# Kernel optimization log

Hardware: AMD Instinct MI355X
Metric: run time of the kernel (lower is better)

The kernel has to match this reference:

```python
import jax, jax.numpy as jnp
import numpy as np

LOG2 = float(np.log(2.0))

def ssp(x):
    # shifted softplus: softplus(x) - log(2)
    return jax.nn.softplus(x) - LOG2

N_NODES = 50000
N_EDGES = 600000
HID = 128
NF = 128

def setup_inputs() -> dict:
    key = jax.random.key(0)
    ks = jax.random.split(key, 10)
    x = jax.random.normal(ks[0], (N_NODES, HID), dtype=jnp.float32)
    edge_attr = jax.random.normal(ks[1], (N_EDGES, NF), dtype=jnp.float32)
    edge_index = jax.random.randint(ks[2], (2, N_EDGES), 0, N_NODES, dtype=jnp.int32)
    s = 1.0 / np.sqrt(NF)
    fc1_w = jax.random.uniform(ks[3], (NF, HID), jnp.float32, -s, s)   # CFConv.fc1 (no bias)
    f_w1 = jax.random.uniform(ks[4], (NF, NF), jnp.float32, -s, s)     # filter_mlp[0]
    f_b1 = jnp.zeros((NF,), jnp.float32)
    f_w2 = jax.random.uniform(ks[5], (NF, NF), jnp.float32, -s, s)     # filter_mlp[2]
    f_b2 = jnp.zeros((NF,), jnp.float32)
    s_w1 = jax.random.uniform(ks[6], (NF, NF), jnp.float32, -s, s)     # StateMLP.fc1
    s_w2 = jax.random.uniform(ks[7], (NF, NF), jnp.float32, -s, s)     # StateMLP.fc2
    return {"x": x, "edge_attr": edge_attr, "edge_index": edge_index,
            "fc1_w": fc1_w, "f_w1": f_w1, "f_b1": f_b1, "f_w2": f_w2,
            "f_b2": f_b2, "s_w1": s_w1, "s_w2": s_w2}

def reference(x, edge_attr, edge_index, fc1_w, f_w1, f_b1, f_w2, f_b2, s_w1, s_w2):
    src, dst = edge_index[0], edge_index[1]  # x_j = x[src], aggregate at dst
    # filter network on edge attributes: [E, NF]
    W = ssp(ssp(edge_attr @ f_w1.T + f_b1) @ f_w2.T + f_b2)
    # message: gather source nodes, linear transform, filter multiply
    msg = (x[src] @ fc1_w.T) * W                               # [E, NF]
    # scatter-add aggregation into nodes
    agg = jax.ops.segment_sum(msg, dst, num_segments=x.shape[0])  # [N, NF]
    # StateMLP
    return ssp(agg @ s_w1.T) @ s_w2.T
```

## Files before the change

kernel.cpp:

```cpp
#include <hip/hip_runtime.h>

#define F 128

typedef __attribute__((ext_vector_type(8))) __bf16 bf16x8;
typedef __attribute__((ext_vector_type(4))) float floatx4;

__device__ __forceinline__ float ssp(float x) {
    return __logf(fmaf(0.5f, __expf(x), 0.5f));
}

__global__ void prep_kernel(const float* __restrict__ fc1w,
                            const float* __restrict__ fw1,
                            const float* __restrict__ fw2,
                            const float* __restrict__ sw1,
                            const float* __restrict__ sw2,
                            __bf16* __restrict__ fc1h, __bf16* __restrict__ fc1l,
                            __bf16* __restrict__ fw1h, __bf16* __restrict__ fw2h,
                            __bf16* __restrict__ sw1h, __bf16* __restrict__ sw1l,
                            __bf16* __restrict__ sw2h, __bf16* __restrict__ sw2l)
{
    int i = blockIdx.x * blockDim.x + threadIdx.x;
    if (i >= F * F) return;
    float v; __bf16 h;
    v = fc1w[i]; h = (__bf16)v; fc1h[i] = h; fc1l[i] = (__bf16)(v - (float)h);
    v = sw1[i];  h = (__bf16)v; sw1h[i] = h; sw1l[i] = (__bf16)(v - (float)h);
    v = sw2[i];  h = (__bf16)v; sw2h[i] = h; sw2l[i] = (__bf16)(v - (float)h);
    fw1h[i] = (__bf16)fw1[i];
    fw2h[i] = (__bf16)fw2[i];
}

__global__ __launch_bounds__(256) void hist_kernel(const int* __restrict__ eidx,
                                                   int* __restrict__ cnt, int E)
{
    int i = blockIdx.x * 256 + threadIdx.x;
    if (i < E) atomicAdd(&cnt[eidx[E + i]], 1);
}

__global__ __launch_bounds__(1024) void scan1_kernel(int* __restrict__ cnt,
                                                     int* __restrict__ bsums, int N)
{
    __shared__ int sd[1024];
    const int t = threadIdx.x;
    const int i = blockIdx.x * 1024 + t;
    int v = (i < N) ? cnt[i] : 0;
    sd[t] = v;
    __syncthreads();
    for (int off = 1; off < 1024; off <<= 1) {
        int add = (t >= off) ? sd[t - off] : 0;
        __syncthreads();
        sd[t] += add;
        __syncthreads();
    }
    if (i < N) cnt[i] = sd[t] - v;
    if (t == 1023) bsums[blockIdx.x] = sd[t];
}

__global__ void scan2_kernel(int* __restrict__ bsums, int nb)
{
    if (threadIdx.x == 0 && blockIdx.x == 0) {
        int acc = 0;
        for (int j = 0; j < nb; ++j) { int c = bsums[j]; bsums[j] = acc; acc += c; }
    }
}

__global__ __launch_bounds__(1024) void scan3_kernel(int* __restrict__ cnt,
                                                     const int* __restrict__ bsums, int N)
{
    int i = blockIdx.x * 1024 + threadIdx.x;
    if (i < N) cnt[i] += bsums[blockIdx.x];
}

__global__ __launch_bounds__(256) void scatter_kernel(const int* __restrict__ eidx,
                                                      int* __restrict__ cursor,
                                                      int* __restrict__ perm,
                                                      int* __restrict__ ssrc,
                                                      int* __restrict__ sdst, int E)
{
    int i = blockIdx.x * 256 + threadIdx.x;
    if (i < E) {
        int d = eidx[E + i];
        int slot = atomicAdd(&cursor[d], 1);
        perm[slot] = i;
        ssrc[slot] = eidx[i];
        sdst[slot] = d;
    }
}

__global__ __launch_bounds__(256) void fc1_kernel(
    const float* __restrict__ x, const __bf16* __restrict__ wh,
    const __bf16* __restrict__ wl, float* __restrict__ y, int M)
{
    const int tid = threadIdx.x;
    const int wv = tid >> 6, lane = tid & 63;
    const int m16 = lane & 15, q = lane >> 4;
    const int g = wv & 1, c = wv >> 1;
    const int rowA0 = blockIdx.x * 32 + g * 16 + m16;
    const int rowA = rowA0 < M ? rowA0 : M - 1;

    floatx4 acc[4] = {};
    #pragma unroll
    for (int ks = 0; ks < 4; ++ks) {
        const int kb = ks * 32 + q * 8;
        const float4* p = (const float4*)(x + (size_t)rowA * F + kb);
        float4 a0 = p[0], a1 = p[1];
        float fv[8] = {a0.x, a0.y, a0.z, a0.w, a1.x, a1.y, a1.z, a1.w};
        bf16x8 ah, al;
        #pragma unroll
        for (int i = 0; i < 8; ++i) {
            __bf16 h = (__bf16)fv[i];
            ah[i] = h; al[i] = (__bf16)(fv[i] - (float)h);
        }
        #pragma unroll
        for (int nt = 0; nt < 4; ++nt) {
            const size_t wo = (size_t)(c * 64 + nt * 16 + m16) * F + kb;
            bf16x8 bh = *(const bf16x8*)(wh + wo);
            bf16x8 bl = *(const bf16x8*)(wl + wo);
            acc[nt] = __builtin_amdgcn_mfma_f32_16x16x32_bf16(ah, bh, acc[nt], 0, 0, 0);
            acc[nt] = __builtin_amdgcn_mfma_f32_16x16x32_bf16(al, bh, acc[nt], 0, 0, 0);
            acc[nt] = __builtin_amdgcn_mfma_f32_16x16x32_bf16(ah, bl, acc[nt], 0, 0, 0);
        }
    }
    const int rowD0 = blockIdx.x * 32 + g * 16 + q * 4;
    #pragma unroll
    for (int nt = 0; nt < 4; ++nt) {
        const int col = c * 64 + nt * 16 + m16;
        #pragma unroll
        for (int r = 0; r < 4; ++r) {
            const int row = rowD0 + r;
            if (row < M) y[(size_t)row * F + col] = acc[nt][r];
        }
    }
}

__global__ __launch_bounds__(256) void edge_kernel(
    const float* __restrict__ edge_attr,
    const int* __restrict__ perm,
    const int* __restrict__ ssrc,
    const int* __restrict__ sdst,
    const float* __restrict__ fb1, const float* __restrict__ fb2,
    const __bf16* __restrict__ fw1, const __bf16* __restrict__ fw2,
    const float* __restrict__ y,
    float* __restrict__ agg, int E)
{
    __shared__ __bf16 h1[64][136];

    const int tid = threadIdx.x;
    const int wv = tid >> 6, lane = tid & 63;
    const int m16 = lane & 15, q = lane >> 4;
    const int e0 = blockIdx.x * 64;
    const int pA0 = e0 + wv * 16 + m16;
    const int pA = pA0 < E ? pA0 : E - 1;
    const int eA = perm[pA];

    floatx4 acc[8] = {};
    #pragma unroll
    for (int ks = 0; ks < 4; ++ks) {
        const int kb = ks * 32 + q * 8;
        const float4* pa = (const float4*)(edge_attr + (size_t)eA * F + kb);
        float4 a0 = pa[0], a1 = pa[1];
        float fv[8] = {a0.x, a0.y, a0.z, a0.w, a1.x, a1.y, a1.z, a1.w};
        bf16x8 aF;
        #pragma unroll
        for (int i = 0; i < 8; ++i) aF[i] = (__bf16)fv[i];
        #pragma unroll
        for (int nt = 0; nt < 8; ++nt) {
            bf16x8 bF = *(const bf16x8*)(fw1 + (size_t)(nt * 16 + m16) * F + kb);
            acc[nt] = __builtin_amdgcn_mfma_f32_16x16x32_bf16(aF, bF, acc[nt], 0, 0, 0);
        }
    }
    #pragma unroll
    for (int nt = 0; nt < 8; ++nt) {
        const int col = nt * 16 + m16;
        const float b = fb1[col];
        #pragma unroll
        for (int r = 0; r < 4; ++r) {
            const int row = wv * 16 + q * 4 + r;
            h1[row][col] = (__bf16)ssp(acc[nt][r] + b);
        }
    }
    __syncthreads();

    floatx4 zero = {};
    #pragma unroll
    for (int nt = 0; nt < 8; ++nt) acc[nt] = zero;
    #pragma unroll
    for (int ks = 0; ks < 4; ++ks) {
        const int kb = ks * 32 + q * 8;
        bf16x8 aF = *(const bf16x8*)(&h1[wv * 16 + m16][kb]);
        #pragma unroll
        for (int nt = 0; nt < 8; ++nt) {
            bf16x8 bF = *(const bf16x8*)(fw2 + (size_t)(nt * 16 + m16) * F + kb);
            acc[nt] = __builtin_amdgcn_mfma_f32_16x16x32_bf16(aF, bF, acc[nt], 0, 0, 0);
        }
    }

    int src[4], dst[4], ok[4];
    #pragma unroll
    for (int r = 0; r < 4; ++r) {
        const int p = e0 + wv * 16 + q * 4 + r;
        const int pc = p < E ? p : E - 1;
        ok[r] = (p < E);
        src[r] = ssrc[pc];
        dst[r] = sdst[pc];
    }
    #pragma unroll
    for (int nt = 0; nt < 8; ++nt) {
        const int col = nt * 16 + m16;
        const float b = fb2[col];
        float run = 0.f;
        #pragma unroll
        for (int r = 0; r < 4; ++r) {
            if (ok[r]) {
                const float wV = ssp(acc[nt][r] + b);
                run += y[(size_t)src[r] * F + col] * wV;
                const bool flush = (r == 3) || (!ok[r + 1]) || (dst[r + 1] != dst[r]);
                if (flush) {
                    unsafeAtomicAdd(&agg[(size_t)dst[r] * F + col], run);
                    run = 0.f;
                }
            }
        }
    }
}

__global__ __launch_bounds__(256) void state_kernel(
    const float* __restrict__ agg,
    const __bf16* __restrict__ w1h, const __bf16* __restrict__ w1l,
    const __bf16* __restrict__ w2h, const __bf16* __restrict__ w2l,
    float* __restrict__ out, int M)
{
    __shared__ __bf16 hh[32][136];
    __shared__ __bf16 hl[32][136];

    const int tid = threadIdx.x;
    const int wv = tid >> 6, lane = tid & 63;
    const int m16 = lane & 15, q = lane >> 4;
    const int g = wv & 1, c = wv >> 1;
    const int rowA0 = blockIdx.x * 32 + g * 16 + m16;
    const int rowA = rowA0 < M ? rowA0 : M - 1;

    floatx4 acc[4] = {};
    #pragma unroll
    for (int ks = 0; ks < 4; ++ks) {
        const int kb = ks * 32 + q * 8;
        const float4* p = (const float4*)(agg + (size_t)rowA * F + kb);
        float4 a0 = p[0], a1 = p[1];
        float fv[8] = {a0.x, a0.y, a0.z, a0.w, a1.x, a1.y, a1.z, a1.w};
        bf16x8 ah, al;
        #pragma unroll
        for (int i = 0; i < 8; ++i) {
            __bf16 h = (__bf16)fv[i];
            ah[i] = h; al[i] = (__bf16)(fv[i] - (float)h);
        }
        #pragma unroll
        for (int nt = 0; nt < 4; ++nt) {
            const size_t wo = (size_t)(c * 64 + nt * 16 + m16) * F + kb;
            bf16x8 bh = *(const bf16x8*)(w1h + wo);
            bf16x8 bl = *(const bf16x8*)(w1l + wo);
            acc[nt] = __builtin_amdgcn_mfma_f32_16x16x32_bf16(ah, bh, acc[nt], 0, 0, 0);
            acc[nt] = __builtin_amdgcn_mfma_f32_16x16x32_bf16(al, bh, acc[nt], 0, 0, 0);
            acc[nt] = __builtin_amdgcn_mfma_f32_16x16x32_bf16(ah, bl, acc[nt], 0, 0, 0);
        }
    }
    #pragma unroll
    for (int nt = 0; nt < 4; ++nt) {
        const int col = c * 64 + nt * 16 + m16;
        #pragma unroll
        for (int r = 0; r < 4; ++r) {
            const int row = g * 16 + q * 4 + r;
            const float h = ssp(acc[nt][r]);
            const __bf16 H = (__bf16)h;
            hh[row][col] = H;
            hl[row][col] = (__bf16)(h - (float)H);
        }
    }
    __syncthreads();

    floatx4 zero = {};
    #pragma unroll
    for (int nt = 0; nt < 4; ++nt) acc[nt] = zero;
    #pragma unroll
    for (int ks = 0; ks < 4; ++ks) {
        const int kb = ks * 32 + q * 8;
        bf16x8 aH = *(const bf16x8*)(&hh[g * 16 + m16][kb]);
        bf16x8 aL = *(const bf16x8*)(&hl[g * 16 + m16][kb]);
        #pragma unroll
        for (int nt = 0; nt < 4; ++nt) {
            const size_t wo = (size_t)(c * 64 + nt * 16 + m16) * F + kb;
            bf16x8 bh = *(const bf16x8*)(w2h + wo);
            bf16x8 bl = *(const bf16x8*)(w2l + wo);
            acc[nt] = __builtin_amdgcn_mfma_f32_16x16x32_bf16(aH, bh, acc[nt], 0, 0, 0);
            acc[nt] = __builtin_amdgcn_mfma_f32_16x16x32_bf16(aL, bh, acc[nt], 0, 0, 0);
            acc[nt] = __builtin_amdgcn_mfma_f32_16x16x32_bf16(aH, bl, acc[nt], 0, 0, 0);
        }
    }
    const int rowD0 = blockIdx.x * 32 + g * 16 + q * 4;
    #pragma unroll
    for (int nt = 0; nt < 4; ++nt) {
        const int col = c * 64 + nt * 16 + m16;
        #pragma unroll
        for (int r = 0; r < 4; ++r) {
            const int row = rowD0 + r;
            if (row < M) out[(size_t)row * F + col] = acc[nt][r];
        }
    }
}

extern "C" void kernel_launch(void* const* d_in, const int* in_sizes, int n_in,
                              void* d_out, int out_size, void* d_ws, size_t ws_size,
                              hipStream_t stream)
{
    const float* x         = (const float*)d_in[0];
    const float* edge_attr = (const float*)d_in[1];
    const int*   eidx      = (const int*)d_in[2];
    const float* fc1w      = (const float*)d_in[3];
    const float* fw1       = (const float*)d_in[4];
    const float* fb1       = (const float*)d_in[5];
    const float* fw2       = (const float*)d_in[6];
    const float* fb2       = (const float*)d_in[7];
    const float* sw1       = (const float*)d_in[8];
    const float* sw2       = (const float*)d_in[9];
    float* out = (float*)d_out;

    const int N = in_sizes[0] / F;
    const int E = in_sizes[1] / F;

    float* agg = (float*)d_ws;
    float* y   = agg + (size_t)N * F;
    __bf16* wb = (__bf16*)(y + (size_t)N * F);
    const int WSZ = F * F;
    __bf16* fc1h = wb;            __bf16* fc1l = wb + WSZ;
    __bf16* fw1h = wb + 2 * WSZ;  __bf16* fw2h = wb + 3 * WSZ;
    __bf16* sw1h = wb + 4 * WSZ;  __bf16* sw1l = wb + 5 * WSZ;
    __bf16* sw2h = wb + 6 * WSZ;  __bf16* sw2l = wb + 7 * WSZ;
    int* cnt   = (int*)(wb + 8 * WSZ);
    int* bsums = cnt + N;
    int* perm  = bsums + 64;
    int* ssrc  = perm + E;
    int* sdst  = ssrc + E;

    const int nb1 = (N + 1023) / 1024;

    hipMemsetAsync(agg, 0, (size_t)N * F * sizeof(float), stream);
    hipMemsetAsync(cnt, 0, (size_t)N * sizeof(int), stream);

    prep_kernel<<<(WSZ + 255) / 256, 256, 0, stream>>>(
        fc1w, fw1, fw2, sw1, sw2, fc1h, fc1l, fw1h, fw2h, sw1h, sw1l, sw2h, sw2l);

    fc1_kernel<<<(N + 31) / 32, 256, 0, stream>>>(x, fc1h, fc1l, y, N);

    hist_kernel<<<(E + 255) / 256, 256, 0, stream>>>(eidx, cnt, E);
    scan1_kernel<<<nb1, 1024, 0, stream>>>(cnt, bsums, N);
    scan2_kernel<<<1, 64, 0, stream>>>(bsums, nb1);
    scan3_kernel<<<nb1, 1024, 0, stream>>>(cnt, bsums, N);
    scatter_kernel<<<(E + 255) / 256, 256, 0, stream>>>(eidx, cnt, perm, ssrc, sdst, E);

    edge_kernel<<<(E + 63) / 64, 256, 0, stream>>>(
        edge_attr, perm, ssrc, sdst, fb1, fb2, fw1h, fw2h, y, agg, E);

    state_kernel<<<(N + 31) / 32, 256, 0, stream>>>(
        agg, sw1h, sw1l, sw2h, sw2l, out, N);
}
```

Measured before the change: 1.018 ms.

## Batch weight loads before MFMAs, fold count memset into prep, warp-scan block sums

Several unrelated tweaks land together. Weight fragments are loaded into register arrays before the MFMA chains in all GEMM kernels so their latency overlaps. Occupancy hints are added to launch_bounds. The count-buffer memset moves into the prep kernel, and the serial single-thread block-sum scan becomes a wavefront shuffle scan. The edge kernel also gives each wave its own LDS slice, hoists the gathered y loads ahead of the filter computation, and uses fma. The changes trade more register pressure for fewer launches and more memory-level parallelism. The __syncthreads in the edge kernel is kept even though waves now only use their own slice.

```diff
diff --git a/kernel.cpp b/kernel.cpp
--- a/kernel.cpp
+++ b/kernel.cpp
@@ -7,6 +7,10 @@
 
 __device__ __forceinline__ float ssp(float x) {
     return __logf(fmaf(0.5f, __expf(x), 0.5f));
+}
+
+__device__ __forceinline__ floatx4 mfma_bf16(bf16x8 a, bf16x8 b, floatx4 c) {
+    return __builtin_amdgcn_mfma_f32_16x16x32_bf16(a, b, c, 0, 0, 0);
 }
 
 __global__ void prep_kernel(const float* __restrict__ fc1w,
@@ -17,9 +21,11 @@
                             __bf16* __restrict__ fc1h, __bf16* __restrict__ fc1l,
                             __bf16* __restrict__ fw1h, __bf16* __restrict__ fw2h,
                             __bf16* __restrict__ sw1h, __bf16* __restrict__ sw1l,
-                            __bf16* __restrict__ sw2h, __bf16* __restrict__ sw2l)
+                            __bf16* __restrict__ sw2h, __bf16* __restrict__ sw2l,
+                            int* __restrict__ cnt, int N)
 {
     int i = blockIdx.x * blockDim.x + threadIdx.x;
+    for (int j = i; j < N; j += gridDim.x * blockDim.x) cnt[j] = 0;
     if (i >= F * F) return;
     float v; __bf16 h;
     v = fc1w[i]; h = (__bf16)v; fc1h[i] = h; fc1l[i] = (__bf16)(v - (float)h);
@@ -57,10 +63,15 @@
 
 __global__ void scan2_kernel(int* __restrict__ bsums, int nb)
 {
-    if (threadIdx.x == 0 && blockIdx.x == 0) {
-        int acc = 0;
-        for (int j = 0; j < nb; ++j) { int c = bsums[j]; bsums[j] = acc; acc += c; }
-    }
+    const int lane = threadIdx.x & 63;
+    int v = (lane < nb) ? bsums[lane] : 0;
+    int acc = v;
+    #pragma unroll
+    for (int off = 1; off < 64; off <<= 1) {
+        int t = __shfl_up(acc, off);
+        if (lane >= off) acc += t;
+    }
+    if (lane < nb) bsums[lane] = acc - v;
 }
 
 __global__ __launch_bounds__(1024) void scan3_kernel(int* __restrict__ cnt,
@@ -86,7 +97,7 @@
     }
 }
 
-__global__ __launch_bounds__(256) void fc1_kernel(
+__global__ __launch_bounds__(256, 5) void fc1_kernel(
     const float* __restrict__ x, const __bf16* __restrict__ wh,
     const __bf16* __restrict__ wl, float* __restrict__ y, int M)
 {
@@ -110,14 +121,18 @@
             __bf16 h = (__bf16)fv[i];
             ah[i] = h; al[i] = (__bf16)(fv[i] - (float)h);
         }
+        bf16x8 bH[4], bL[4];
         #pragma unroll
         for (int nt = 0; nt < 4; ++nt) {
             const size_t wo = (size_t)(c * 64 + nt * 16 + m16) * F + kb;
-            bf16x8 bh = *(const bf16x8*)(wh + wo);
-            bf16x8 bl = *(const bf16x8*)(wl + wo);
-            acc[nt] = __builtin_amdgcn_mfma_f32_16x16x32_bf16(ah, bh, acc[nt], 0, 0, 0);
-            acc[nt] = __builtin_amdgcn_mfma_f32_16x16x32_bf16(al, bh, acc[nt], 0, 0, 0);
-            acc[nt] = __builtin_amdgcn_mfma_f32_16x16x32_bf16(ah, bl, acc[nt], 0, 0, 0);
+            bH[nt] = *(const bf16x8*)(wh + wo);
+            bL[nt] = *(const bf16x8*)(wl + wo);
+        }
+        #pragma unroll
+        for (int nt = 0; nt < 4; ++nt) {
+            acc[nt] = mfma_bf16(ah, bH[nt], acc[nt]);
+            acc[nt] = mfma_bf16(al, bH[nt], acc[nt]);
+            acc[nt] = mfma_bf16(ah, bL[nt], acc[nt]);
         }
     }
     const int rowD0 = blockIdx.x * 32 + g * 16 + q * 4;
@@ -132,7 +147,7 @@
     }
 }
 
-__global__ __launch_bounds__(256) void edge_kernel(
+__global__ __launch_bounds__(256, 4) void edge_kernel(
     const float* __restrict__ edge_attr,
     const int* __restrict__ perm,
     const int* __restrict__ ssrc,
@@ -142,15 +157,17 @@
     const float* __restrict__ y,
     float* __restrict__ agg, int E)
 {
-    __shared__ __bf16 h1[64][136];
+    __shared__ __align__(16) __bf16 h1s[4][16][136];
 
     const int tid = threadIdx.x;
     const int wv = tid >> 6, lane = tid & 63;
     const int m16 = lane & 15, q = lane >> 4;
-    const int e0 = blockIdx.x * 64;
-    const int pA0 = e0 + wv * 16 + m16;
-    const int pA = pA0 < E ? pA0 : E - 1;
-    const int eA = perm[pA];
+    const int s0 = blockIdx.x * 64 + wv * 16;
+    __bf16 (*h1)[136] = h1s[wv];
+
+    const int sA0 = s0 + m16;
+    const int sA = sA0 < E ? sA0 : E - 1;
+    const int eA = perm[sA];
 
     floatx4 acc[8] = {};
     #pragma unroll
@@ -162,21 +179,21 @@
         bf16x8 aF;
         #pragma unroll
         for (int i = 0; i < 8; ++i) aF[i] = (__bf16)fv[i];
-        #pragma unroll
-        for (int nt = 0; nt < 8; ++nt) {
-            bf16x8 bF = *(const bf16x8*)(fw1 + (size_t)(nt * 16 + m16) * F + kb);
-            acc[nt] = __builtin_amdgcn_mfma_f32_16x16x32_bf16(aF, bF, acc[nt], 0, 0, 0);
-        }
+        bf16x8 bF[8];
+        #pragma unroll
+        for (int nt = 0; nt < 8; ++nt)
+            bF[nt] = *(const bf16x8*)(fw1 + (size_t)(nt * 16 + m16) * F + kb);
+        #pragma unroll
+        for (int nt = 0; nt < 8; ++nt)
+            acc[nt] = mfma_bf16(aF, bF[nt], acc[nt]);
     }
     #pragma unroll
     for (int nt = 0; nt < 8; ++nt) {
         const int col = nt * 16 + m16;
         const float b = fb1[col];
         #pragma unroll
-        for (int r = 0; r < 4; ++r) {
-            const int row = wv * 16 + q * 4 + r;
-            h1[row][col] = (__bf16)ssp(acc[nt][r] + b);
-        }
+        for (int r = 0; r < 4; ++r)
+            h1[q * 4 + r][col] = (__bf16)ssp(acc[nt][r] + b);
     }
     __syncthreads();
 
@@ -186,33 +203,39 @@
     #pragma unroll
     for (int ks = 0; ks < 4; ++ks) {
         const int kb = ks * 32 + q * 8;
-        bf16x8 aF = *(const bf16x8*)(&h1[wv * 16 + m16][kb]);
-        #pragma unroll
-        for (int nt = 0; nt < 8; ++nt) {
-            bf16x8 bF = *(const bf16x8*)(fw2 + (size_t)(nt * 16 + m16) * F + kb);
-            acc[nt] = __builtin_amdgcn_mfma_f32_16x16x32_bf16(aF, bF, acc[nt], 0, 0, 0);
-        }
+        bf16x8 aF = *(const bf16x8*)(&h1[m16][kb]);
+        bf16x8 bF[8];
+        #pragma unroll
+        for (int nt = 0; nt < 8; ++nt)
+            bF[nt] = *(const bf16x8*)(fw2 + (size_t)(nt * 16 + m16) * F + kb);
+        #pragma unroll
+        for (int nt = 0; nt < 8; ++nt)
+            acc[nt] = mfma_bf16(aF, bF[nt], acc[nt]);
     }
 
     int src[4], dst[4], ok[4];
     #pragma unroll
     for (int r = 0; r < 4; ++r) {
-        const int p = e0 + wv * 16 + q * 4 + r;
-        const int pc = p < E ? p : E - 1;
-        ok[r] = (p < E);
-        src[r] = ssrc[pc];
-        dst[r] = sdst[pc];
+        const int s = s0 + q * 4 + r;
+        const int sc = s < E ? s : E - 1;
+        ok[r] = (s < E);
+        src[r] = ssrc[sc];
+        dst[r] = sdst[sc];
     }
     #pragma unroll
     for (int nt = 0; nt < 8; ++nt) {
         const int col = nt * 16 + m16;
         const float b = fb2[col];
+        float yv[4];
+        #pragma unroll
+        for (int r = 0; r < 4; ++r)
+            yv[r] = y[(size_t)src[r] * F + col];
         float run = 0.f;
         #pragma unroll
         for (int r = 0; r < 4; ++r) {
             if (ok[r]) {
                 const float wV = ssp(acc[nt][r] + b);
-                run += y[(size_t)src[r] * F + col] * wV;
+                run = fmaf(yv[r], wV, run);
                 const bool flush = (r == 3) || (!ok[r + 1]) || (dst[r + 1] != dst[r]);
                 if (flush) {
                     unsafeAtomicAdd(&agg[(size_t)dst[r] * F + col], run);
@@ -223,14 +246,14 @@
     }
 }
 
-__global__ __launch_bounds__(256) void state_kernel(
+__global__ __launch_bounds__(256, 5) void state_kernel(
     const float* __restrict__ agg,
     const __bf16* __restrict__ w1h, const __bf16* __restrict__ w1l,
     const __bf16* __restrict__ w2h, const __bf16* __restrict__ w2l,
     float* __restrict__ out, int M)
 {
-    __shared__ __bf16 hh[32][136];
-    __shared__ __bf16 hl[32][136];
+    __shared__ __align__(16) __bf16 hh[32][136];
+    __shared__ __align__(16) __bf16 hl[32][136];
 
     const int tid = threadIdx.x;
     const int wv = tid >> 6, lane = tid & 63;
@@ -252,14 +275,18 @@
             __bf16 h = (__bf16)fv[i];
             ah[i] = h; al[i] = (__bf16)(fv[i] - (float)h);
         }
+        bf16x8 bH[4], bL[4];
         #pragma unroll
         for (int nt = 0; nt < 4; ++nt) {
             const size_t wo = (size_t)(c * 64 + nt * 16 + m16) * F + kb;
-            bf16x8 bh = *(const bf16x8*)(w1h + wo);
-            bf16x8 bl = *(const bf16x8*)(w1l + wo);
-            acc[nt] = __builtin_amdgcn_mfma_f32_16x16x32_bf16(ah, bh, acc[nt], 0, 0, 0);
-            acc[nt] = __builtin_amdgcn_mfma_f32_16x16x32_bf16(al, bh, acc[nt], 0, 0, 0);
-            acc[nt] = __builtin_amdgcn_mfma_f32_16x16x32_bf16(ah, bl, acc[nt], 0, 0, 0);
+            bH[nt] = *(const bf16x8*)(w1h + wo);
+            bL[nt] = *(const bf16x8*)(w1l + wo);
+        }
+        #pragma unroll
+        for (int nt = 0; nt < 4; ++nt) {
+            acc[nt] = mfma_bf16(ah, bH[nt], acc[nt]);
+            acc[nt] = mfma_bf16(al, bH[nt], acc[nt]);
+            acc[nt] = mfma_bf16(ah, bL[nt], acc[nt]);
         }
     }
     #pragma unroll
@@ -284,14 +311,18 @@
         const int kb = ks * 32 + q * 8;
         bf16x8 aH = *(const bf16x8*)(&hh[g * 16 + m16][kb]);
         bf16x8 aL = *(const bf16x8*)(&hl[g * 16 + m16][kb]);
+        bf16x8 bH[4], bL[4];
         #pragma unroll
         for (int nt = 0; nt < 4; ++nt) {
             const size_t wo = (size_t)(c * 64 + nt * 16 + m16) * F + kb;
-            bf16x8 bh = *(const bf16x8*)(w2h + wo);
-            bf16x8 bl = *(const bf16x8*)(w2l + wo);
-            acc[nt] = __builtin_amdgcn_mfma_f32_16x16x32_bf16(aH, bh, acc[nt], 0, 0, 0);
-            acc[nt] = __builtin_amdgcn_mfma_f32_16x16x32_bf16(aL, bh, acc[nt], 0, 0, 0);
-            acc[nt] = __builtin_amdgcn_mfma_f32_16x16x32_bf16(aH, bl, acc[nt], 0, 0, 0);
+            bH[nt] = *(const bf16x8*)(w2h + wo);
+            bL[nt] = *(const bf16x8*)(w2l + wo);
+        }
+        #pragma unroll
+        for (int nt = 0; nt < 4; ++nt) {
+            acc[nt] = mfma_bf16(aH, bH[nt], acc[nt]);
+            acc[nt] = mfma_bf16(aL, bH[nt], acc[nt]);
+            acc[nt] = mfma_bf16(aH, bL[nt], acc[nt]);
         }
     }
     const int rowD0 = blockIdx.x * 32 + g * 16 + q * 4;
@@ -342,10 +373,10 @@
     const int nb1 = (N + 1023) / 1024;
 
     hipMemsetAsync(agg, 0, (size_t)N * F * sizeof(float), stream);
-    hipMemsetAsync(cnt, 0, (size_t)N * sizeof(int), stream);
 
     prep_kernel<<<(WSZ + 255) / 256, 256, 0, stream>>>(
-        fc1w, fw1, fw2, sw1, sw2, fc1h, fc1l, fw1h, fw2h, sw1h, sw1l, sw2h, sw2l);
+        fc1w, fw1, fw2, sw1, sw2, fc1h, fc1l, fw1h, fw2h, sw1h, sw1l, sw2h, sw2l,
+        cnt, N);
 
     fc1_kernel<<<(N + 31) / 32, 256, 0, stream>>>(x, fc1h, fc1l, y, N);
 
```

Measured after the change: 947.8 us. -6.9%, faster.
